# Kernel tuning notes

Hardware: AMD Instinct MI355X
Metric: run time of the kernel (lower is better)

## Reference

```python
import jax, jax.numpy as jnp
import numpy as np

D = 1024; H = 16; N = 64; F = 4096
B = 1; T = 2048
W_LORA = 64; A_LORA = 64; V_LORA = 32; G_LORA = 128


def rmsnorm(x, w, eps=1e-6):
    x32 = x.astype(jnp.float32)
    var = jnp.mean(x32 * x32, axis=-1, keepdims=True)
    return w * (x32 * jax.lax.rsqrt(var + eps))


def rwkv7_scan(r, w_log, k, v, a, b, state):
    # r,w_log,k,v,a,b: [B,T,H,N]; state: [B,H,N,N] (value dim, key dim)
    decay = jnp.exp(w_log)  # kernel applies exp to the log-decay w = -exp(w_pre)
    def step(S, inp):
        r_t, d_t, k_t, v_t, a_t, b_t = inp  # each [B,H,N]
        sa = jnp.einsum('bhij,bhj->bhi', S, a_t)
        S = S * d_t[:, :, None, :] + sa[..., None] * b_t[:, :, None, :] + v_t[..., None] * k_t[:, :, None, :]
        o_t = jnp.einsum('bhij,bhj->bhi', S, r_t)
        return S, o_t
    seq = tuple(jnp.moveaxis(t, 1, 0) for t in (r, decay, k, v, a, b))  # [T,B,H,N]
    state_f, o = jax.lax.scan(step, state, seq)
    return jnp.moveaxis(o, 0, 1), state_f  # [B,T,H,N], [B,H,N,N]


def setup_inputs() -> dict:
    key = jax.random.key(0)
    ks = iter(jax.random.split(key, 64))
    def nrm(shape, s=1.0):
        return jax.random.normal(next(ks), shape, dtype=jnp.float32) * s
    def uni(shape):
        return jax.random.uniform(next(ks), shape, dtype=jnp.float32)
    WS = 0.02  # weight scale for big matrices
    inp = {
        'x': nrm((B, T, D)),
        'x_prev': nrm((B, D)),
        'v_first': nrm((B, T, D)),
        'state': jnp.zeros((B, H, N, N), jnp.float32),
        'ln1_w': jnp.ones((D,), jnp.float32),
        'ln2_w': jnp.ones((D,), jnp.float32),
        'x_r': uni((1, 1, D)), 'x_w': uni((1, 1, D)), 'x_k': uni((1, 1, D)),
        'x_v': uni((1, 1, D)), 'x_a': uni((1, 1, D)), 'x_g': uni((1, 1, D)),
        'w0': nrm((1, 1, D), 0.5), 'w1': nrm((D, W_LORA), WS), 'w2': nrm((W_LORA, D), WS),
        'a0': nrm((1, 1, D), 0.1), 'a1': nrm((D, A_LORA), WS), 'a2': nrm((A_LORA, D), WS),
        'v0': nrm((1, 1, D), 0.1), 'v1': nrm((D, V_LORA), WS), 'v2': nrm((V_LORA, D), WS),
        'g1': nrm((D, G_LORA), WS), 'g2': nrm((G_LORA, D), WS),
        'k_k': uni((D,)), 'k_a': uni((D,)), 'r_k': nrm((D,), 0.1),
        'R_': nrm((D, D), WS), 'K_': nrm((D, D), WS), 'V_': nrm((D, D), WS), 'O_': nrm((D, D), WS),
        'gate_w': nrm((D, F), WS), 'up_w': nrm((D, F), WS), 'down_w': nrm((F, D), WS),
    }
    return inp


def _block(x, x_prev, v_first, state, ln1_w, ln2_w, x_r, x_w, x_k, x_v, x_a, x_g,
           w0, w1, w2, a0, a1, a2, v0, v1, v2, g1, g2, k_k, k_a, r_k,
           R_, K_, V_, O_, gate_w, up_w, down_w):
    Bx, Tx, _ = x.shape
    xn = rmsnorm(x, ln1_w)  # ln1
    # token shift
    xx = jnp.concatenate([x_prev[:, None, :], xn[:, :-1]], axis=1) - xn
    xr = xn + xx * x_r; xw = xn + xx * x_w; xk = xn + xx * x_k
    xv = xn + xx * x_v; xa = xn + xx * x_a; xg = xn + xx * x_g
    r = xr @ R_
    w_pre = -jax.nn.softplus(-(w0 + jnp.tanh(xw @ w1) @ w2)) - 0.5
    k = xk @ K_
    v = xv @ V_
    a = jax.nn.sigmoid(a0 + (xa @ a1) @ a2)
    g = jax.nn.sigmoid(xg @ g1) @ g2
    kk = (k * k_k).reshape(Bx, Tx, H, N)
    kk = kk / jnp.maximum(jnp.linalg.norm(kk, axis=-1, keepdims=True), 1e-12)
    kk = kk.reshape(Bx, Tx, H * N)
    k = k * (1 + (a - 1) * k_a)
    # layer_id > 0: lerp toward v_first
    v = v + (v_first - v) * jax.nn.sigmoid(v0 + (xv @ v1) @ v2)
    w_log = -jnp.exp(w_pre)  # log-decay passed to the recurrent kernel
    aa = -kk
    bb = kk * a
    hv = lambda t: t.reshape(Bx, Tx, H, N)
    o, state_f = rwkv7_scan(hv(r), hv(w_log), hv(k), hv(v), hv(aa), hv(bb), state)
    o = o.reshape(Bx, Tx, H * N)
    bonus = ((r * k * r_k).reshape(Bx, Tx, H, N).sum(-1, keepdims=True) * v.reshape(Bx, Tx, H, N)).reshape(Bx, Tx, H * N)
    o = o + bonus
    x = x + (o * g) @ O_
    # SwiGLU MLP
    xm = rmsnorm(x, ln2_w)
    x = x + (jax.nn.silu(xm @ gate_w) * (xm @ up_w)) @ down_w
    return x, xn[:, -1], state_f


def reference(x, x_prev, v_first, state, ln1_w, ln2_w, x_r, x_w, x_k, x_v, x_a, x_g,
              w0, w1, w2, a0, a1, a2, v0, v1, v2, g1, g2, k_k, k_a, r_k,
              R_, K_, V_, O_, gate_w, up_w, down_w):
    return _block(x, x_prev, v_first, state, ln1_w, ln2_w, x_r, x_w, x_k, x_v, x_a, x_g,
                  w0, w1, w2, a0, a1, a2, v0, v1, v2, g1, g2, k_k, k_a, r_k,
                  R_, K_, V_, O_, gate_w, up_w, down_w)
```

## Files before the change

kernel.cpp:

```cpp
#include <hip/hip_runtime.h>
#include <math.h>

#define T_ 2048
#define D_ 1024
#define H_ 16
#define N_ 64
#define F_ 4096
#define NCHUNK 64
#define CLEN 32

typedef __attribute__((ext_vector_type(8))) short bf16x8;
typedef __attribute__((ext_vector_type(4))) float f32x4;
typedef __attribute__((address_space(3))) unsigned int lds_u32_t;
typedef __attribute__((address_space(1))) const unsigned int glb_u32_t;

static __device__ __forceinline__ float sigf(float x) { return 1.0f / (1.0f + __expf(-x)); }

static __device__ __forceinline__ ushort f2bf(float f) {
    union { float f; unsigned u; } c; c.f = f;
    unsigned r = (c.u + 0x7FFFu + ((c.u >> 16) & 1u)) >> 16;
    return (ushort)r;
}
static __device__ __forceinline__ float bf2f(ushort h) {
    union { unsigned u; float f; } c; c.u = ((unsigned)h) << 16;
    return c.f;
}

static __device__ __forceinline__ void st4(float* p, float4 v) { *(float4*)p = v; }
static __device__ __forceinline__ void st4(ushort* p, float4 v) {
    ushort4 o; o.x = f2bf(v.x); o.y = f2bf(v.y); o.z = f2bf(v.z); o.w = f2bf(v.w);
    *(ushort4*)p = o;
}

template <typename OutT>
__global__ __launch_bounds__(256) void rmsnorm_kernel(const float* __restrict__ x,
                                                      const float* __restrict__ w,
                                                      OutT* __restrict__ out,
                                                      float* __restrict__ last) {
    const int t = blockIdx.x;
    const int tid = threadIdx.x;
    const float4* xr = (const float4*)(x + (size_t)t * D_);
    float4 v = xr[tid];
    float ss = v.x * v.x + v.y * v.y + v.z * v.z + v.w * v.w;
    ss += __shfl_xor(ss, 1);
    ss += __shfl_xor(ss, 2);
    ss += __shfl_xor(ss, 4);
    ss += __shfl_xor(ss, 8);
    ss += __shfl_xor(ss, 16);
    ss += __shfl_xor(ss, 32);
    __shared__ float red[4];
    if ((tid & 63) == 0) red[tid >> 6] = ss;
    __syncthreads();
    float tot = red[0] + red[1] + red[2] + red[3];
    float scale = rsqrtf(tot * (1.0f / (float)D_) + 1e-6f);
    float4 wv = ((const float4*)w)[tid];
    float4 o;
    o.x = wv.x * v.x * scale;
    o.y = wv.y * v.y * scale;
    o.z = wv.z * v.z * scale;
    o.w = wv.w * v.w * scale;
    st4(out + (size_t)t * D_ + tid * 4, o);
    if (last != nullptr && t == T_ - 1) ((float4*)last)[tid] = o;
}

__global__ __launch_bounds__(256) void rmsnorm_reduce2(
    const float* __restrict__ x, const float* __restrict__ p0, const float* __restrict__ p1,
    const float* __restrict__ w, float* __restrict__ resid_out, ushort* __restrict__ xm) {
    const int t = blockIdx.x;
    const int tid = threadIdx.x;
    const size_t base = (size_t)t * D_ + tid * 4;
    float4 v = *(const float4*)(x + base);
    float4 a = *(const float4*)(p0 + base);
    float4 b = *(const float4*)(p1 + base);
    v.x += a.x + b.x; v.y += a.y + b.y; v.z += a.z + b.z; v.w += a.w + b.w;
    st4(resid_out + base, v);
    float ss = v.x * v.x + v.y * v.y + v.z * v.z + v.w * v.w;
    ss += __shfl_xor(ss, 1);
    ss += __shfl_xor(ss, 2);
    ss += __shfl_xor(ss, 4);
    ss += __shfl_xor(ss, 8);
    ss += __shfl_xor(ss, 16);
    ss += __shfl_xor(ss, 32);
    __shared__ float red[4];
    if ((tid & 63) == 0) red[tid >> 6] = ss;
    __syncthreads();
    float tot = red[0] + red[1] + red[2] + red[3];
    float scale = rsqrtf(tot * (1.0f / (float)D_) + 1e-6f);
    float4 wv = ((const float4*)w)[tid];
    float4 o;
    o.x = wv.x * v.x * scale;
    o.y = wv.y * v.y * scale;
    o.z = wv.z * v.z * scale;
    o.w = wv.w * v.w * scale;
    st4(xm + base, o);
}

__global__ __launch_bounds__(256) void add4_kernel(float* __restrict__ out,
                                                   const float* __restrict__ p,
                                                   int n4slice) {
    const int i = blockIdx.x * 256 + threadIdx.x;
    const float4* p4 = (const float4*)p;
    float4 o = ((const float4*)out)[i];
    float4 a = p4[i], b = p4[i + n4slice], c = p4[i + 2 * n4slice], d = p4[i + 3 * n4slice];
    o.x += (a.x + b.x) + (c.x + d.x);
    o.y += (a.y + b.y) + (c.y + d.y);
    o.z += (a.z + b.z) + (c.z + d.z);
    o.w += (a.w + b.w) + (c.w + d.w);
    ((float4*)out)[i] = o;
}

__global__ __launch_bounds__(256) void shift_kernel(
    const float* __restrict__ xn, const float* __restrict__ x_prev,
    const float* __restrict__ cr, const float* __restrict__ cw, const float* __restrict__ ck,
    const float* __restrict__ cv, const float* __restrict__ ca, const float* __restrict__ cg,
    ushort* __restrict__ xr, ushort* __restrict__ xw, ushort* __restrict__ xk,
    ushort* __restrict__ xv, ushort* __restrict__ xa, ushort* __restrict__ xg) {
    const int i = blockIdx.x * 256 + threadIdx.x;
    const int t = i >> 8, j = i & 255;
    const float4* xn4 = (const float4*)xn;
    float4 cur = xn4[i];
    float4 prev = (t == 0) ? ((const float4*)x_prev)[j] : xn4[i - 256];
    float4 xx;
    xx.x = prev.x - cur.x;
    xx.y = prev.y - cur.y;
    xx.z = prev.z - cur.z;
    xx.w = prev.w - cur.w;
#define APPLY(dst, c)                                   \
    {                                                   \
        float4 cc = ((const float4*)c)[j];              \
        float4 o;                                       \
        o.x = cur.x + xx.x * cc.x;                      \
        o.y = cur.y + xx.y * cc.y;                      \
        o.z = cur.z + xx.z * cc.z;                      \
        o.w = cur.w + xx.w * cc.w;                      \
        st4(dst + (size_t)i * 4, o);                    \
    }
    APPLY(xr, cr)
    APPLY(xw, cw)
    APPLY(xk, ck)
    APPLY(xv, cv)
    APPLY(xa, ca)
    APPLY(xg, cg)
#undef APPLY
}

struct TDesc { const float* in; ushort* out; int K, N, off; };
struct TPack { TDesc d[15]; };

__global__ __launch_bounds__(256) void transpose_cast_multi(TPack p) {
    __shared__ float tile[32][33];
    const int bid = blockIdx.x;
    int di = 0;
#pragma unroll
    for (int i = 1; i < 15; i++)
        if (bid >= p.d[i].off) di = i;
    const TDesc d = p.d[di];
    const int local = bid - d.off;
    const int nt = d.N >> 5;
    const int bx = local % nt, by = local / nt;
    const int tx = threadIdx.x & 31, ty = threadIdx.x >> 5;
    const int n0 = bx * 32, k0 = by * 32;
#pragma unroll
    for (int i = 0; i < 4; i++)
        tile[ty + i * 8][tx] = d.in[(size_t)(k0 + ty + i * 8) * d.N + n0 + tx];
    __syncthreads();
#pragma unroll
    for (int i = 0; i < 4; i++)
        d.out[(size_t)(n0 + ty + i * 8) * d.K + k0 + tx] = f2bf(tile[tx][ty + i * 8]);
}

template <typename OutT, bool PARTIAL>
__global__ __launch_bounds__(256) void mfma_gemm(
    const ushort* __restrict__ A, const ushort* __restrict__ BT, OutT* __restrict__ C,
    const float* res, int M, int Ntot, int K, int klen, int epi) {
    __shared__ ushort As[2][128 * 32];
    __shared__ ushort Bs[2][128 * 32];
    const int tid = threadIdx.x;
    const int wave = tid >> 6, lane = tid & 63;
    const int wr = wave >> 1, wc = wave & 1;
    const int lrow = lane & 15, quad = lane >> 4;
    int bx = blockIdx.x, by = blockIdx.y;
    if (gridDim.x == 8 && gridDim.y == 16) {
        const int bid = by * 8 + bx;
        const int k = bid & 7, i = bid >> 3;
        bx = ((k & 1) << 2) + (i & 3);
        by = ((k >> 1) << 2) + (i >> 2);
    }
    const int m0 = by * 128, n0 = bx * 128;
    const int kbase = blockIdx.z * klen;
    const int srow = lane >> 2;
    const int scol = (lane & 3) << 3;

    f32x4 acc[4][4] = {};

    auto stage = [&](int buf, int kk) {
#pragma unroll
        for (int j = 0; j < 2; j++) {
            const int chunk = 2 * wave + j;
            const ushort* ga = A + (size_t)(m0 + chunk * 16 + srow) * K + kk + scol;
            __builtin_amdgcn_global_load_lds((glb_u32_t*)ga,
                                             (lds_u32_t*)&As[buf][chunk * 512], 16, 0, 0);
            const int brow = n0 + chunk * 16 + srow;
            if (brow < Ntot) {
                const ushort* gb = BT + (size_t)brow * K + kk + scol;
                __builtin_amdgcn_global_load_lds((glb_u32_t*)gb,
                                                 (lds_u32_t*)&Bs[buf][chunk * 512], 16, 0, 0);
            }
        }
    };

    stage(0, kbase);
    __syncthreads();
    int cur = 0;
    for (int k0 = kbase; k0 < kbase + klen; k0 += 32) {
        if (k0 + 32 < kbase + klen) stage(cur ^ 1, k0 + 32);
        bf16x8 af[4], bfr[4];
#pragma unroll
        for (int mi = 0; mi < 4; mi++)
            af[mi] = *(const bf16x8*)&As[cur][(wr * 64 + mi * 16 + lrow) * 32 + quad * 8];
#pragma unroll
        for (int ni = 0; ni < 4; ni++)
            bfr[ni] = *(const bf16x8*)&Bs[cur][(wc * 64 + ni * 16 + lrow) * 32 + quad * 8];
#pragma unroll
        for (int mi = 0; mi < 4; mi++)
#pragma unroll
            for (int ni = 0; ni < 4; ni++)
                acc[mi][ni] = __builtin_amdgcn_mfma_f32_16x16x32_bf16(af[mi], bfr[ni], acc[mi][ni], 0, 0, 0);
        __syncthreads();
        cur ^= 1;
    }

    const size_t zoff = PARTIAL ? (size_t)blockIdx.z * M * Ntot : 0;
#pragma unroll
    for (int mi = 0; mi < 4; mi++) {
#pragma unroll
        for (int r = 0; r < 4; r++) {
            const int row = m0 + wr * 64 + mi * 16 + quad * 4 + r;
#pragma unroll
            for (int ni = 0; ni < 4; ni++) {
                const int col = n0 + wc * 64 + ni * 16 + lrow;
                if (col < Ntot) {
                    const size_t idx = (size_t)row * Ntot + col;
                    float val = acc[mi][ni][r];
                    if constexpr (PARTIAL) {
                        ((float*)C)[idx + zoff] = val;
                    } else {
                        if (epi == 1) val += res[idx];
                        if constexpr (sizeof(OutT) == 2) C[idx] = (OutT)f2bf(val);
                        else C[idx] = (OutT)val;
                    }
                }
            }
        }
    }
}

struct MMDesc {
    const ushort* A; const ushort* BT;
    float* Cf; ushort* Cb;
    const float* res; const float* res2; const float* bias;
    int Ntot, K, epi;
};
template <int NZ>
struct MMPack { MMDesc d[NZ]; };

template <int NZ>
__global__ __launch_bounds__(256) void mfma_gemm_multi(MMPack<NZ> p) {
    const MMDesc d = p.d[blockIdx.z];
    const int n0 = blockIdx.x * 128;
    if (n0 >= d.Ntot) return;
    __shared__ ushort As[2][128 * 32];
    __shared__ ushort Bs[2][128 * 32];
    const int tid = threadIdx.x;
    const int wave = tid >> 6, lane = tid & 63;
    const int wr = wave >> 1, wc = wave & 1;
    const int lrow = lane & 15, quad = lane >> 4;
    const int m0 = blockIdx.y * 128;
    const int srow = lane >> 2;
    const int scol = (lane & 3) << 3;
    const int K = d.K, Ntot = d.Ntot;

    f32x4 acc[4][4] = {};

    auto stage = [&](int buf, int kk) {
#pragma unroll
        for (int j = 0; j < 2; j++) {
            const int chunk = 2 * wave + j;
            const ushort* ga = d.A + (size_t)(m0 + chunk * 16 + srow) * K + kk + scol;
            __builtin_amdgcn_global_load_lds((glb_u32_t*)ga,
                                             (lds_u32_t*)&As[buf][chunk * 512], 16, 0, 0);
            const int brow = n0 + chunk * 16 + srow;
            if (brow < Ntot) {
                const ushort* gb = d.BT + (size_t)brow * K + kk + scol;
                __builtin_amdgcn_global_load_lds((glb_u32_t*)gb,
                                                 (lds_u32_t*)&Bs[buf][chunk * 512], 16, 0, 0);
            }
        }
    };

    stage(0, 0);
    __syncthreads();
    int cur = 0;
    for (int k0 = 0; k0 < K; k0 += 32) {
        if (k0 + 32 < K) stage(cur ^ 1, k0 + 32);
        bf16x8 af[4], bfr[4];
#pragma unroll
        for (int mi = 0; mi < 4; mi++)
            af[mi] = *(const bf16x8*)&As[cur][(wr * 64 + mi * 16 + lrow) * 32 + quad * 8];
#pragma unroll
        for (int ni = 0; ni < 4; ni++)
            bfr[ni] = *(const bf16x8*)&Bs[cur][(wc * 64 + ni * 16 + lrow) * 32 + quad * 8];
#pragma unroll
        for (int mi = 0; mi < 4; mi++)
#pragma unroll
            for (int ni = 0; ni < 4; ni++)
                acc[mi][ni] = __builtin_amdgcn_mfma_f32_16x16x32_bf16(af[mi], bfr[ni], acc[mi][ni], 0, 0, 0);
        __syncthreads();
        cur ^= 1;
    }

#pragma unroll
    for (int mi = 0; mi < 4; mi++) {
#pragma unroll
        for (int r = 0; r < 4; r++) {
            const int row = m0 + wr * 64 + mi * 16 + quad * 4 + r;
#pragma unroll
            for (int ni = 0; ni < 4; ni++) {
                const int col = n0 + wc * 64 + ni * 16 + lrow;
                if (col < Ntot) {
                    const size_t idx = (size_t)row * Ntot + col;
                    float val = acc[mi][ni][r];
                    switch (d.epi) {
                        case 3: val = tanhf(val); break;
                        case 4: val = sigf(val); break;
                        case 5: val = sigf(d.bias[col] + val); break;
                        case 6: val = __expf(-0.60653065971263342f * sigf(d.bias[col] + val)); break;
                        case 7: {
                            float vr = d.res[idx];
                            val = vr + (d.res2[idx] - vr) * sigf(d.bias[col] + val);
                        } break;
                        default: break;
                    }
                    if (d.Cb) d.Cb[idx] = f2bf(val);
                    else d.Cf[idx] = val;
                }
            }
        }
    }
}

__global__ __launch_bounds__(256) void kk_kernel(float* __restrict__ k,
                                                 const float* __restrict__ a_sig,
                                                 const float* __restrict__ k_k,
                                                 const float* __restrict__ k_a,
                                                 float* __restrict__ kk,
                                                 float* __restrict__ mb) {
    const int b = blockIdx.x * 4 + (threadIdx.x >> 6);
    const int t = b >> 4, h = b & 15;
    const int lane = threadIdx.x & 63;
    const size_t idx = (size_t)t * D_ + h * N_ + lane;
    const int wi = h * N_ + lane;
    const float kraw = k[idx];
    const float kv = kraw * k_k[wi];
    float ss = kv * kv;
    ss += __shfl_xor(ss, 1);
    ss += __shfl_xor(ss, 2);
    ss += __shfl_xor(ss, 4);
    ss += __shfl_xor(ss, 8);
    ss += __shfl_xor(ss, 16);
    ss += __shfl_xor(ss, 32);
    const float nrm = fmaxf(sqrtf(ss), 1e-12f);
    const float kkn = kv / nrm;
    kk[idx] = kkn;
    mb[idx] = -kkn * a_sig[idx];
    k[idx] = kraw * (1.0f + (a_sig[idx] - 1.0f) * k_a[wi]);
}

#define FOR16(M) M(0) M(1) M(2) M(3) M(4) M(5) M(6) M(7) \
                 M(8) M(9) M(10) M(11) M(12) M(13) M(14) M(15)

__global__ __launch_bounds__(64, 1) void scan_pass1(
    const float* __restrict__ gR, const float* __restrict__ gD, const float* __restrict__ gK,
    const float* __restrict__ gV, const float* __restrict__ gKK, const float* __restrict__ gMB,
    float* __restrict__ Pbuf, float* __restrict__ Lbuf,
    float* __restrict__ zbuf, float* __restrict__ olbuf) {
    const int bid = blockIdx.x;
    const int h = bid & 15;
    const int c = bid >> 4;
    const int lane = threadIdx.x;
    const int hb = h * N_;
    const int t0 = c * CLEN;
    const int tend = t0 + CLEN - 1;

    __shared__ __align__(16) unsigned char ring[2 * 2048];

    const int rsel = lane >> 4;
    const int sub4 = (lane & 15) << 2;
    const float* p1 = (rsel == 0 ? gR : rsel == 1 ? gD : rsel == 2 ? gK : gKK)
                      + (size_t)t0 * D_ + hb + sub4;
    const float* p2 = (rsel == 1 ? gV : gMB) + (size_t)t0 * D_ + hb + sub4;

#define DECLP(q) f32x4 sp##q = {(lane == 4 * q + 0) ? 1.0f : 0.0f, \
                                (lane == 4 * q + 1) ? 1.0f : 0.0f, \
                                (lane == 4 * q + 2) ? 1.0f : 0.0f, \
                                (lane == 4 * q + 3) ? 1.0f : 0.0f};
    FOR16(DECLP)
#undef DECLP
#define DECLL(q) f32x4 sl##q = {0.f, 0.f, 0.f, 0.f};
    FOR16(DECLL)
#undef DECLL

    float4 r0a, r0b, r1a, r1b, r2a, r2b, r3a, r3b;

#define LOADQ(qa, qb, tt) {                                                  \
        const size_t _adv = (size_t)((tt) - t0) * D_;                        \
        qa = *(const float4*)(p1 + _adv);                                    \
        qb = *(const float4*)(p2 + _adv); }
#define WRITEQ(sl, qa, qb) {                                                 \
        *(float4*)(ring + (sl) * 2048 + lane * 16) = qa;                     \
        *(float4*)(ring + (sl) * 2048 + 1024 + lane * 16) = qb; }
#define PA(q) { const f32x4 kk4 = sKKr[q];                                   \
        pacc += sp##q * kk4; lacc += sl##q * kk4; }
#define PB(q) {                                                   \
        const f32x4 d4 = sDr[q];                                  \
        const f32x4 k4 = sKr[q];                                  \
        const f32x4 m4 = sMBr[q];                                 \
        const f32x4 r4 = sRr[q];                                  \
        sp##q = sp##q * d4 + m4 * sapP;                           \
        sl##q = sl##q * d4 + (m4 * sapL + k4 * vv);               \
        oP += sp##q * r4;                                         \
        oL += sl##q * r4;                                         \
    }
#define COMPUTE(sl, tt) {                                                    \
        const unsigned char* sb = (const unsigned char*)ring + (sl) * 2048;  \
        const f32x4* sRr = (const f32x4*)(sb);                               \
        const f32x4* sDr = (const f32x4*)(sb + 256);                         \
        const f32x4* sKr = (const f32x4*)(sb + 512);                         \
        const f32x4* sKKr = (const f32x4*)(sb + 768);                        \
        const f32x4* sMBr = (const f32x4*)(sb + 1024);                       \
        const float* sVr = (const float*)(sb + 1280);                        \
        f32x4 pacc = {0.f, 0.f, 0.f, 0.f};                                   \
        f32x4 lacc = {0.f, 0.f, 0.f, 0.f};                                   \
        FOR16(PA)                                                            \
        const float sapP = (pacc.x + pacc.y) + (pacc.z + pacc.w);            \
        const float sapL = (lacc.x + lacc.y) + (lacc.z + lacc.w);            \
        const float vv = sVr[lane];                                          \
        f32x4 oP = {0.f, 0.f, 0.f, 0.f};                                     \
        f32x4 oL = {0.f, 0.f, 0.f, 0.f};                                     \
        FOR16(PB)                                                            \
        zbuf[(size_t)(tt) * D_ + hb + lane] = (oP.x + oP.y) + (oP.z + oP.w); \
        olbuf[(size_t)(tt) * D_ + hb + lane] = (oL.x + oL.y) + (oL.z + oL.w); }

    LOADQ(r0a, r0b, t0)
    LOADQ(r1a, r1b, t0 + 1)
    LOADQ(r2a, r2b, t0 + 2)
    LOADQ(r3a, r3b, t0 + 3)
    WRITEQ(0, r0a, r0b)

    for (int t = t0; t < t0 + CLEN; t += 4) {
        WRITEQ(1, r1a, r1b)
        LOADQ(r0a, r0b, (t + 4 > tend ? tend : t + 4))
        COMPUTE(0, t)
        WRITEQ(0, r2a, r2b)
        LOADQ(r1a, r1b, (t + 5 > tend ? tend : t + 5))
        COMPUTE(1, t + 1)
        WRITEQ(1, r3a, r3b)
        LOADQ(r2a, r2b, (t + 6 > tend ? tend : t + 6))
        COMPUTE(0, t + 2)
        WRITEQ(0, r0a, r0b)
        LOADQ(r3a, r3b, (t + 7 > tend ? tend : t + 7))
        COMPUTE(1, t + 3)
    }
#undef COMPUTE
#undef PB
#undef PA
#undef WRITEQ
#undef LOADQ

    const size_t base = ((size_t)c * 16 + h) * 4096 + (size_t)lane * 64;
#define STP(q) *(f32x4*)(Pbuf + base + 4 * q) = sp##q;
    FOR16(STP)
#undef STP
#define STL(q) *(f32x4*)(Lbuf + base + 4 * q) = sl##q;
    FOR16(STL)
#undef STL
}

__global__ __launch_bounds__(64) void merge_pairs(float* __restrict__ Pbuf,
                                                  float* __restrict__ Lbuf) {
    const int h = blockIdx.x & 15, j = blockIdx.x >> 4;
    const int t = threadIdx.x;
    __shared__ float PaT[64][65];
    __shared__ float LaT[64][65];
    __shared__ float Pb[64][68];
    const size_t ca = ((size_t)(2 * j) * 16 + h) * 4096;
    const size_t cb = ((size_t)(2 * j + 1) * 16 + h) * 4096;
#pragma unroll
    for (int q = 0; q < 16; q++) {
        const int idx = t + q * 64;
        const int r = idx >> 4, c4 = (idx & 15) << 2;
        float4 pa = *(const float4*)(Pbuf + ca + (size_t)r * 64 + c4);
        float4 la = *(const float4*)(Lbuf + ca + (size_t)r * 64 + c4);
        float4 pb = *(const float4*)(Pbuf + cb + (size_t)r * 64 + c4);
        PaT[c4 + 0][r] = pa.x; PaT[c4 + 1][r] = pa.y;
        PaT[c4 + 2][r] = pa.z; PaT[c4 + 3][r] = pa.w;
        LaT[c4 + 0][r] = la.x; LaT[c4 + 1][r] = la.y;
        LaT[c4 + 2][r] = la.z; LaT[c4 + 3][r] = la.w;
        *(float4*)&Pb[r][c4] = pb;
    }
    __syncthreads();
    const int cg = (t & 3) << 4;
    const int r0 = (t >> 2) << 2;
    float4 accP[4][4] = {};
    float4 accL[4][4];
#pragma unroll
    for (int rr = 0; rr < 4; rr++)
#pragma unroll
        for (int e = 0; e < 4; e++)
            accL[rr][e] = *(const float4*)(Lbuf + cb + (size_t)(r0 + rr) * 64 + cg + 4 * e);
    for (int m = 0; m < 64; m++) {
        float4 pb4[4];
#pragma unroll
        for (int e = 0; e < 4; e++) pb4[e] = *(const float4*)&Pb[m][cg + 4 * e];
#pragma unroll
        for (int rr = 0; rr < 4; rr++) {
            const float pa = PaT[m][r0 + rr];
            const float la = LaT[m][r0 + rr];
#pragma unroll
            for (int e = 0; e < 4; e++) {
                accP[rr][e].x = fmaf(pa, pb4[e].x, accP[rr][e].x);
                accP[rr][e].y = fmaf(pa, pb4[e].y, accP[rr][e].y);
                accP[rr][e].z = fmaf(pa, pb4[e].z, accP[rr][e].z);
                accP[rr][e].w = fmaf(pa, pb4[e].w, accP[rr][e].w);
                accL[rr][e].x = fmaf(la, pb4[e].x, accL[rr][e].x);
                accL[rr][e].y = fmaf(la, pb4[e].y, accL[rr][e].y);
                accL[rr][e].z = fmaf(la, pb4[e].z, accL[rr][e].z);
                accL[rr][e].w = fmaf(la, pb4[e].w, accL[rr][e].w);
            }
        }
    }
#pragma unroll
    for (int rr = 0; rr < 4; rr++)
#pragma unroll
        for (int e = 0; e < 4; e++) {
            *(float4*)(Pbuf + cb + (size_t)(r0 + rr) * 64 + cg + 4 * e) = accP[rr][e];
            *(float4*)(Lbuf + cb + (size_t)(r0 + rr) * 64 + cg + 4 * e) = accL[rr][e];
        }
}

__global__ __launch_bounds__(256) void scan_combine(
    const float* __restrict__ state_in, const float* __restrict__ Pbuf,
    const float* __restrict__ Lbuf, float* __restrict__ SstT, float* __restrict__ state_out) {
    const int h = blockIdx.x >> 2, rg = blockIdx.x & 3;
    const int tid = threadIdx.x;
    const int i = tid >> 4, j4 = (tid & 15) << 2;
    const int gi = rg * 16 + i;
    __shared__ float Sl[16][68];
    __shared__ float Pl[64][68];

    float4 sv = *(const float4*)(state_in + (size_t)h * 4096 + gi * 64 + j4);
    *(float4*)&Sl[i][j4] = sv;

    float4 rp0, rp1, rp2, rp3, rl;
    {
        const size_t cb = ((size_t)1 * 16 + h) * 4096;
        rp0 = *(const float4*)(Pbuf + cb + (size_t)(i +  0) * 64 + j4);
        rp1 = *(const float4*)(Pbuf + cb + (size_t)(i + 16) * 64 + j4);
        rp2 = *(const float4*)(Pbuf + cb + (size_t)(i + 32) * 64 + j4);
        rp3 = *(const float4*)(Pbuf + cb + (size_t)(i + 48) * 64 + j4);
        rl  = *(const float4*)(Lbuf + cb + (size_t)gi * 64 + j4);
    }
    __syncthreads();

    for (int c = 0; c < NCHUNK / 2; c++) {
        *(float4*)&Pl[i +  0][j4] = rp0;
        *(float4*)&Pl[i + 16][j4] = rp1;
        *(float4*)&Pl[i + 32][j4] = rp2;
        *(float4*)&Pl[i + 48][j4] = rp3;
        float4 acc = rl;
        const size_t so = ((size_t)(2 * c) * 16 + h) * 4096;
        float4 scur = *(const float4*)&Sl[i][j4];
        SstT[so + (size_t)(j4 + 0) * 64 + gi] = scur.x;
        SstT[so + (size_t)(j4 + 1) * 64 + gi] = scur.y;
        SstT[so + (size_t)(j4 + 2) * 64 + gi] = scur.z;
        SstT[so + (size_t)(j4 + 3) * 64 + gi] = scur.w;
        __syncthreads();
        if (c + 1 < NCHUNK / 2) {
            const size_t cb = ((size_t)(2 * c + 3) * 16 + h) * 4096;
            rp0 = *(const float4*)(Pbuf + cb + (size_t)(i +  0) * 64 + j4);
            rp1 = *(const float4*)(Pbuf + cb + (size_t)(i + 16) * 64 + j4);
            rp2 = *(const float4*)(Pbuf + cb + (size_t)(i + 32) * 64 + j4);
            rp3 = *(const float4*)(Pbuf + cb + (size_t)(i + 48) * 64 + j4);
            rl  = *(const float4*)(Lbuf + cb + (size_t)gi * 64 + j4);
        }
#pragma unroll 8
        for (int m = 0; m < 64; m++) {
            const float smv = Sl[i][m];
            const float4 p4 = *(const float4*)&Pl[m][j4];
            acc.x = fmaf(smv, p4.x, acc.x);
            acc.y = fmaf(smv, p4.y, acc.y);
            acc.z = fmaf(smv, p4.z, acc.z);
            acc.w = fmaf(smv, p4.w, acc.w);
        }
        __syncthreads();
        *(float4*)&Sl[i][j4] = acc;
    }
    *(float4*)(state_out + (size_t)h * 4096 + gi * 64 + j4) = *(const float4*)&Sl[i][j4];
}

__global__ __launch_bounds__(256) void scan_oddfill(
    const float* __restrict__ Pbuf, const float* __restrict__ Lbuf,
    float* __restrict__ SstT) {
    const int b = blockIdx.x;
    const int rg = b & 3, h = (b >> 2) & 15, j = b >> 6;
    const int tid = threadIdx.x;
    const int i = tid >> 4, j4 = (tid & 15) << 2;
    const int gi = rg * 16 + i;
    __shared__ float Sl[16][68];
    __shared__ float Pl[64][68];
    const size_t ce = ((size_t)(2 * j) * 16 + h) * 4096;
    const size_t co = ((size_t)(2 * j + 1) * 16 + h) * 4096;
    {
        float4 s;
        s.x = SstT[ce + (size_t)(j4 + 0) * 64 + gi];
        s.y = SstT[ce + (size_t)(j4 + 1) * 64 + gi];
        s.z = SstT[ce + (size_t)(j4 + 2) * 64 + gi];
        s.w = SstT[ce + (size_t)(j4 + 3) * 64 + gi];
        *(float4*)&Sl[i][j4] = s;
    }
#pragma unroll
    for (int q = 0; q < 4; q++) {
        const int prq = i + q * 16;
        *(float4*)&Pl[prq][j4] = *(const float4*)(Pbuf + ce + (size_t)prq * 64 + j4);
    }
    __syncthreads();
    float4 acc = *(const float4*)(Lbuf + ce + (size_t)gi * 64 + j4);
#pragma unroll 8
    for (int m = 0; m < 64; m++) {
        const float smv = Sl[i][m];
        const float4 p4 = *(const float4*)&Pl[m][j4];
        acc.x = fmaf(smv, p4.x, acc.x);
        acc.y = fmaf(smv, p4.y, acc.y);
        acc.z = fmaf(smv, p4.z, acc.z);
        acc.w = fmaf(smv, p4.w, acc.w);
    }
    SstT[co + (size_t)(j4 + 0) * 64 + gi] = acc.x;
    SstT[co + (size_t)(j4 + 1) * 64 + gi] = acc.y;
    SstT[co + (size_t)(j4 + 2) * 64 + gi] = acc.z;
    SstT[co + (size_t)(j4 + 3) * 64 + gi] = acc.w;
}

__global__ __launch_bounds__(256) void scan_fix(
    const float* __restrict__ zbuf, const float* __restrict__ olbuf,
    const float* __restrict__ SstT, float* __restrict__ o) {
    const int tg = blockIdx.x >> 4, h = blockIdx.x & 15;
    const int hb = h * N_;
    const int tid = threadIdx.x;
    const int tok = tid >> 4, i4 = (tid & 15) << 2;
    const int tbase = tg * 16;
    const int c = tbase / CLEN;
    __shared__ float zl[16][68];
    __shared__ float Sl[64][68];

    *(float4*)&zl[tok][i4] = *(const float4*)(zbuf + (size_t)(tbase + tok) * D_ + hb + i4);
    const size_t cb = ((size_t)c * 16 + h) * 4096;
#pragma unroll
    for (int q = 0; q < 4; q++) {
        const int jr = (tid >> 4) + q * 16;
        *(float4*)&Sl[jr][i4] = *(const float4*)(SstT + cb + (size_t)jr * 64 + i4);
    }
    __syncthreads();
    float4 acc = *(const float4*)(olbuf + (size_t)(tbase + tok) * D_ + hb + i4);
#pragma unroll 8
    for (int j = 0; j < 64; j++) {
        const float zv = zl[tok][j];
        const float4 p4 = *(const float4*)&Sl[j][i4];
        acc.x = fmaf(zv, p4.x, acc.x);
        acc.y = fmaf(zv, p4.y, acc.y);
        acc.z = fmaf(zv, p4.z, acc.z);
        acc.w = fmaf(zv, p4.w, acc.w);
    }
    *(float4*)(o + (size_t)(tbase + tok) * D_ + hb + i4) = acc;
}

__global__ __launch_bounds__(256) void bonus_kernel(const float* __restrict__ o,
                                                    const float* __restrict__ r,
                                                    const float* __restrict__ k,
                                                    const float* __restrict__ v,
                                                    const float* __restrict__ g,
                                                    const float* __restrict__ r_k,
                                                    ushort* __restrict__ og) {
    const int b = blockIdx.x * 4 + (threadIdx.x >> 6);
    const int t = b >> 4, h = b & 15;
    const int lane = threadIdx.x & 63;
    const size_t idx = (size_t)t * D_ + h * N_ + lane;
    float c = r[idx] * k[idx] * r_k[h * N_ + lane];
    c += __shfl_xor(c, 1);
    c += __shfl_xor(c, 2);
    c += __shfl_xor(c, 4);
    c += __shfl_xor(c, 8);
    c += __shfl_xor(c, 16);
    c += __shfl_xor(c, 32);
    const float on = o[idx] + c * v[idx];
    og[idx] = f2bf(on * g[idx]);
}

__global__ __launch_bounds__(256) void mulz_kernel(const ushort* __restrict__ Z,
                                                   ushort* __restrict__ Hb) {
    const int idx = blockIdx.x * 256 + threadIdx.x;
    const int t = idx >> 10;
    const int j = (idx & 1023) << 2;
    const ushort4 zg = *(const ushort4*)(Z + (size_t)t * 8192 + j);
    const ushort4 zu = *(const ushort4*)(Z + (size_t)t * 8192 + 4096 + j);
    ushort4 o;
    float g0 = bf2f(zg.x), g1 = bf2f(zg.y), g2 = bf2f(zg.z), g3 = bf2f(zg.w);
    o.x = f2bf(g0 * sigf(g0) * bf2f(zu.x));
    o.y = f2bf(g1 * sigf(g1) * bf2f(zu.y));
    o.z = f2bf(g2 * sigf(g2) * bf2f(zu.z));
    o.w = f2bf(g3 * sigf(g3) * bf2f(zu.w));
    *(ushort4*)(Hb + (size_t)t * 4096 + j) = o;
}

extern "C" void kernel_launch(void* const* d_in, const int* in_sizes, int n_in,
                              void* d_out, int out_size, void* d_ws, size_t ws_size,
                              hipStream_t stream) {
    const float* x      = (const float*)d_in[0];
    const float* x_prev = (const float*)d_in[1];
    const float* v_first= (const float*)d_in[2];
    const float* state  = (const float*)d_in[3];
    const float* ln1_w  = (const float*)d_in[4];
    const float* ln2_w  = (const float*)d_in[5];
    const float* x_r    = (const float*)d_in[6];
    const float* x_w    = (const float*)d_in[7];
    const float* x_k    = (const float*)d_in[8];
    const float* x_v    = (const float*)d_in[9];
    const float* x_a    = (const float*)d_in[10];
    const float* x_g    = (const float*)d_in[11];
    const float* w0     = (const float*)d_in[12];
    const float* w1     = (const float*)d_in[13];
    const float* w2     = (const float*)d_in[14];
    const float* a0     = (const float*)d_in[15];
    const float* a1     = (const float*)d_in[16];
    const float* a2     = (const float*)d_in[17];
    const float* v0     = (const float*)d_in[18];
    const float* v1     = (const float*)d_in[19];
    const float* v2     = (const float*)d_in[20];
    const float* g1     = (const float*)d_in[21];
    const float* g2     = (const float*)d_in[22];
    const float* k_k    = (const float*)d_in[23];
    const float* k_a    = (const float*)d_in[24];
    const float* r_k    = (const float*)d_in[25];
    const float* R_     = (const float*)d_in[26];
    const float* K_     = (const float*)d_in[27];
    const float* V_     = (const float*)d_in[28];
    const float* O_     = (const float*)d_in[29];
    const float* gate_w = (const float*)d_in[30];
    const float* up_w   = (const float*)d_in[31];
    const float* down_w = (const float*)d_in[32];

    float* ws = (float*)d_ws;
    const size_t U = (size_t)T_ * D_;
    float* u_r  = ws;
    float* u_k  = ws + 1 * U;
    float* u_v  = ws + 2 * U;
    float* u_dc = ws + 3 * U;
    float* u_kk = ws + 4 * U;
    float* u_mb = ws + 5 * U;
    float* u_g  = ws + 6 * U;
    float* u_ao = ws + 7 * U;
    ushort* XB = (ushort*)(ws + 8 * U);
    const size_t TD = U;
    ushort* XR = XB + 0 * TD;
    ushort* XW = XB + 1 * TD;
    ushort* XK = XB + 2 * TD;
    ushort* XV = XB + 3 * TD;
    ushort* XA = XB + 4 * TD;
    ushort* XG = XB + 5 * TD;
    float* Pbuf  = (float*)XB;
    float* Lbuf  = u_g;
    float* zbuf  = ws + 10 * U;
    float* olbuf = (float*)d_out;
    float* SstT  = u_dc;
    float* obuf  = u_mb;
    ushort* OG   = XB;
    ushort* XM   = (ushort*)(ws + 10 * U);
    float* Opart = ws + 4 * U;
    ushort* Zbuf = (ushort*)ws;
    ushort* Hbuf = (ushort*)(ws + 4 * U);
    float* Dpart = ws;
    ushort* WT = (ushort*)(ws + 11 * U);
    const size_t DD = (size_t)D_ * D_;
    const size_t DF = (size_t)D_ * F_;
    ushort* WTR = WT;
    ushort* WTK = WTR + DD;
    ushort* WTV = WTK + DD;
    ushort* WTO = WTV + DD;
    ushort* WTG = WTO + DD;
    ushort* WTU = WTG + DF;
    ushort* WTD = WTU + DF;
    ushort* WTw1 = WTD + DF;
    ushort* WTw2 = WTw1 + 64 * 1024;
    ushort* WTa1 = WTw2 + 64 * 1024;
    ushort* WTa2 = WTa1 + 64 * 1024;
    ushort* WTv1 = WTa2 + 64 * 1024;
    ushort* WTv2 = WTv1 + 32 * 1024;
    ushort* WTg1 = WTv2 + 32 * 1024;
    ushort* WTg2 = WTg1 + 128 * 1024;
    ushort* Lw = WTg2 + 128 * 1024;
    ushort* La = Lw + (size_t)T_ * 64;
    ushort* Lv = La + (size_t)T_ * 64;
    ushort* Lg = Lv + (size_t)T_ * 32;

    float* out_x = (float*)d_out;
    float* out_xn_last = out_x + (size_t)T_ * D_;
    float* out_state = out_xn_last + D_;

    TPack tp;
    int toff = 0, ti = 0;
    auto addT = [&](const float* in, ushort* out, int K, int N) {
        tp.d[ti].in = in; tp.d[ti].out = out; tp.d[ti].K = K; tp.d[ti].N = N; tp.d[ti].off = toff;
        toff += (N / 32) * (K / 32); ++ti;
    };
    addT(R_, WTR, D_, D_);
    addT(K_, WTK, D_, D_);
    addT(V_, WTV, D_, D_);
    addT(O_, WTO, D_, D_);
    addT(gate_w, WTG, D_, F_);
    addT(up_w, WTU, D_, F_);
    addT(down_w, WTD, F_, D_);
    addT(w1, WTw1, D_, 64);
    addT(w2, WTw2, 64, D_);
    addT(a1, WTa1, D_, 64);
    addT(a2, WTa2, 64, D_);
    addT(v1, WTv1, D_, 32);
    addT(v2, WTv2, 32, D_);
    addT(g1, WTg1, D_, 128);
    addT(g2, WTg2, 128, D_);
    transpose_cast_multi<<<toff, 256, 0, stream>>>(tp);

    rmsnorm_kernel<float><<<T_, 256, 0, stream>>>(x, ln1_w, out_x, out_xn_last);
    shift_kernel<<<T_, 256, 0, stream>>>(out_x, x_prev, x_r, x_w, x_k, x_v, x_a, x_g,
                                         XR, XW, XK, XV, XA, XG);
    auto mkmm = [](const ushort* A, const ushort* BT, float* Cf, ushort* Cb,
                   const float* res, const float* res2, const float* bias,
                   int Ntot, int K, int epi) {
        MMDesc m{A, BT, Cf, Cb, res, res2, bias, Ntot, K, epi};
        return m;
    };
    MMPack<7> pa;
    pa.d[0] = mkmm(XR, WTR, u_r, nullptr, nullptr, nullptr, nullptr, D_, D_, 0);
    pa.d[1] = mkmm(XK, WTK, u_k, nullptr, nullptr, nullptr, nullptr, D_, D_, 0);
    pa.d[2] = mkmm(XV, WTV, u_v, nullptr, nullptr, nullptr, nullptr, D_, D_, 0);
    pa.d[3] = mkmm(XW, WTw1, nullptr, Lw, nullptr, nullptr, nullptr, 64,  D_, 3);
    pa.d[4] = mkmm(XA, WTa1, nullptr, La, nullptr, nullptr, nullptr, 64,  D_, 0);
    pa.d[5] = mkmm(XV, WTv1, nullptr, Lv, nullptr, nullptr, nullptr, 32,  D_, 0);
    pa.d[6] = mkmm(XG, WTg1, nullptr, Lg, nullptr, nullptr, nullptr, 128, D_, 4);
    mfma_gemm_multi<7><<<dim3(8, 16, 7), 256, 0, stream>>>(pa);
    MMPack<3> pb;
    pb.d[0] = mkmm(Lw, WTw2, u_dc, nullptr, nullptr, nullptr, w0, D_, 64,  6);
    pb.d[1] = mkmm(La, WTa2, u_ao, nullptr, nullptr, nullptr, a0, D_, 64,  5);
    pb.d[2] = mkmm(Lv, WTv2, u_v,  nullptr, u_v, v_first,     v0, D_, 32,  7);
    mfma_gemm_multi<3><<<dim3(8, 16, 3), 256, 0, stream>>>(pb);
    kk_kernel<<<T_ * H_ / 4, 256, 0, stream>>>(u_k, u_ao, k_k, k_a, u_kk, u_mb);
    scan_pass1<<<NCHUNK * H_, 64, 0, stream>>>(u_r, u_dc, u_k, u_v, u_kk, u_mb,
                                               Pbuf, Lbuf, zbuf, olbuf);
    merge_pairs<<<16 * 32, 64, 0, stream>>>(Pbuf, Lbuf);
    scan_combine<<<H_ * 4, 256, 0, stream>>>(state, Pbuf, Lbuf, SstT, out_state);
    scan_oddfill<<<16 * 32 * 4, 256, 0, stream>>>(Pbuf, Lbuf, SstT);
    mfma_gemm<float, false><<<dim3(8, 16), 256, 0, stream>>>(
        Lg, WTg2, u_g, nullptr, T_, D_, 128, 128, 0);
    scan_fix<<<(T_ / 16) * H_, 256, 0, stream>>>(zbuf, olbuf, SstT, obuf);
    bonus_kernel<<<T_ * H_ / 4, 256, 0, stream>>>(obuf, u_r, u_k, u_v, u_g, r_k, OG);
    mfma_gemm<float, true><<<dim3(8, 16, 2), 256, 0, stream>>>(
        OG, WTO, Opart, nullptr, T_, D_, D_, 512, 0);
    rmsnorm_reduce2<<<T_, 256, 0, stream>>>(x, Opart, Opart + U, ln2_w, out_x, XM);
    mfma_gemm<ushort, false><<<dim3(64, 16), 256, 0, stream>>>(
        XM, WTG, Zbuf, nullptr, T_, 2 * F_, D_, D_, 0);
    mulz_kernel<<<(T_ * (F_ / 4)) / 256, 256, 0, stream>>>(Zbuf, Hbuf);
    mfma_gemm<float, true><<<dim3(8, 16, 4), 256, 0, stream>>>(
        Hbuf, WTD, Dpart, nullptr, T_, D_, F_, 1024, 0);
    add4_kernel<<<(int)(U / 4 / 256), 256, 0, stream>>>(out_x, Dpart, (int)(U / 4));
}
```

Measured before the change: 620.1 us.

## Fuse rmsnorm with token shift, bonus into scan_fix, and SwiGLU into GEMM epilogue

Merges the first rmsnorm and the token-shift kernel into one kernel that recomputes the previous token's norm instead of reading it back. The bonus/gating pass moves into scan_fix, and the gate/up weights are interleaved in 16-column groups so the fused gate-up GEMM can apply silu(g)*u in its epilogue and write the hidden activations directly. This removes three launches and the round trips through the large intermediate Z buffer and the o buffer, at the cost of doing the previous-row norm twice and a more involved GEMM epilogue and weight layout.

Result: no change. 612.6 us (-1.2%).

```diff
diff --git a/kernel.cpp b/kernel.cpp
--- a/kernel.cpp
+++ b/kernel.cpp
@@ -32,35 +32,66 @@
     *(ushort4*)p = o;
 }
 
-template <typename OutT>
-__global__ __launch_bounds__(256) void rmsnorm_kernel(const float* __restrict__ x,
-                                                      const float* __restrict__ w,
-                                                      OutT* __restrict__ out,
-                                                      float* __restrict__ last) {
+__global__ __launch_bounds__(256) void ln_shift_kernel(
+    const float* __restrict__ x, const float* __restrict__ x_prev,
+    const float* __restrict__ w,
+    const float* __restrict__ cr, const float* __restrict__ cw, const float* __restrict__ ck,
+    const float* __restrict__ cv, const float* __restrict__ ca, const float* __restrict__ cg,
+    ushort* __restrict__ xr, ushort* __restrict__ xw, ushort* __restrict__ xk,
+    ushort* __restrict__ xv, ushort* __restrict__ xa, ushort* __restrict__ xg,
+    float* __restrict__ last) {
     const int t = blockIdx.x;
     const int tid = threadIdx.x;
-    const float4* xr = (const float4*)(x + (size_t)t * D_);
-    float4 v = xr[tid];
-    float ss = v.x * v.x + v.y * v.y + v.z * v.z + v.w * v.w;
-    ss += __shfl_xor(ss, 1);
-    ss += __shfl_xor(ss, 2);
-    ss += __shfl_xor(ss, 4);
-    ss += __shfl_xor(ss, 8);
-    ss += __shfl_xor(ss, 16);
-    ss += __shfl_xor(ss, 32);
-    __shared__ float red[4];
-    if ((tid & 63) == 0) red[tid >> 6] = ss;
+    const float4* x4 = (const float4*)x;
+    float4 xc = x4[t * 256 + tid];
+    float4 xp = (t == 0) ? ((const float4*)x_prev)[tid] : x4[(t - 1) * 256 + tid];
+    float ssc = xc.x * xc.x + xc.y * xc.y + xc.z * xc.z + xc.w * xc.w;
+    float ssp = xp.x * xp.x + xp.y * xp.y + xp.z * xp.z + xp.w * xp.w;
+    ssc += __shfl_xor(ssc, 1); ssp += __shfl_xor(ssp, 1);
+    ssc += __shfl_xor(ssc, 2); ssp += __shfl_xor(ssp, 2);
+    ssc += __shfl_xor(ssc, 4); ssp += __shfl_xor(ssp, 4);
+    ssc += __shfl_xor(ssc, 8); ssp += __shfl_xor(ssp, 8);
+    ssc += __shfl_xor(ssc, 16); ssp += __shfl_xor(ssp, 16);
+    ssc += __shfl_xor(ssc, 32); ssp += __shfl_xor(ssp, 32);
+    __shared__ float redc[4], redp[4];
+    if ((tid & 63) == 0) { redc[tid >> 6] = ssc; redp[tid >> 6] = ssp; }
     __syncthreads();
-    float tot = red[0] + red[1] + red[2] + red[3];
-    float scale = rsqrtf(tot * (1.0f / (float)D_) + 1e-6f);
+    const float totc = redc[0] + redc[1] + redc[2] + redc[3];
+    const float totp = redp[0] + redp[1] + redp[2] + redp[3];
+    const float sc = rsqrtf(totc * (1.0f / (float)D_) + 1e-6f);
+    const float sp = rsqrtf(totp * (1.0f / (float)D_) + 1e-6f);
     float4 wv = ((const float4*)w)[tid];
-    float4 o;
-    o.x = wv.x * v.x * scale;
-    o.y = wv.y * v.y * scale;
-    o.z = wv.z * v.z * scale;
-    o.w = wv.w * v.w * scale;
-    st4(out + (size_t)t * D_ + tid * 4, o);
-    if (last != nullptr && t == T_ - 1) ((float4*)last)[tid] = o;
+    float4 cur, prev;
+    cur.x = wv.x * xc.x * sc; cur.y = wv.y * xc.y * sc;
+    cur.z = wv.z * xc.z * sc; cur.w = wv.w * xc.w * sc;
+    if (t == 0) {
+        prev = xp;
+    } else {
+        prev.x = wv.x * xp.x * sp; prev.y = wv.y * xp.y * sp;
+        prev.z = wv.z * xp.z * sp; prev.w = wv.w * xp.w * sp;
+    }
+    float4 xx;
+    xx.x = prev.x - cur.x; xx.y = prev.y - cur.y;
+    xx.z = prev.z - cur.z; xx.w = prev.w - cur.w;
+    const size_t ob = (size_t)t * D_ + tid * 4;
+#define APPLY(dst, c)                                   \
+    {                                                   \
+        float4 cc = ((const float4*)c)[tid];            \
+        float4 o;                                       \
+        o.x = cur.x + xx.x * cc.x;                      \
+        o.y = cur.y + xx.y * cc.y;                      \
+        o.z = cur.z + xx.z * cc.z;                      \
+        o.w = cur.w + xx.w * cc.w;                      \
+        st4(dst + ob, o);                               \
+    }
+    APPLY(xr, cr)
+    APPLY(xw, cw)
+    APPLY(xk, ck)
+    APPLY(xv, cv)
+    APPLY(xa, ca)
+    APPLY(xg, cg)
+#undef APPLY
+    if (t == T_ - 1) ((float4*)last)[tid] = cur;
 }
 
 __global__ __launch_bounds__(256) void rmsnorm_reduce2(
@@ -109,42 +140,7 @@
     ((float4*)out)[i] = o;
 }
 
-__global__ __launch_bounds__(256) void shift_kernel(
-    const float* __restrict__ xn, const float* __restrict__ x_prev,
-    const float* __restrict__ cr, const float* __restrict__ cw, const float* __restrict__ ck,
-    const float* __restrict__ cv, const float* __restrict__ ca, const float* __restrict__ cg,
-    ushort* __restrict__ xr, ushort* __restrict__ xw, ushort* __restrict__ xk,
-    ushort* __restrict__ xv, ushort* __restrict__ xa, ushort* __restrict__ xg) {
-    const int i = blockIdx.x * 256 + threadIdx.x;
-    const int t = i >> 8, j = i & 255;
-    const float4* xn4 = (const float4*)xn;
-    float4 cur = xn4[i];
-    float4 prev = (t == 0) ? ((const float4*)x_prev)[j] : xn4[i - 256];
-    float4 xx;
-    xx.x = prev.x - cur.x;
-    xx.y = prev.y - cur.y;
-    xx.z = prev.z - cur.z;
-    xx.w = prev.w - cur.w;
-#define APPLY(dst, c)                                   \
-    {                                                   \
-        float4 cc = ((const float4*)c)[j];              \
-        float4 o;                                       \
-        o.x = cur.x + xx.x * cc.x;                      \
-        o.y = cur.y + xx.y * cc.y;                      \
-        o.z = cur.z + xx.z * cc.z;                      \
-        o.w = cur.w + xx.w * cc.w;                      \
-        st4(dst + (size_t)i * 4, o);                    \
-    }
-    APPLY(xr, cr)
-    APPLY(xw, cw)
-    APPLY(xk, ck)
-    APPLY(xv, cv)
-    APPLY(xa, ca)
-    APPLY(xg, cg)
-#undef APPLY
-}
-
-struct TDesc { const float* in; ushort* out; int K, N, off; };
+struct TDesc { const float* in; ushort* out; int K, N, off, mode; };
 struct TPack { TDesc d[15]; };
 
 __global__ __launch_bounds__(256) void transpose_cast_multi(TPack p) {
@@ -165,8 +161,13 @@
         tile[ty + i * 8][tx] = d.in[(size_t)(k0 + ty + i * 8) * d.N + n0 + tx];
     __syncthreads();
 #pragma unroll
-    for (int i = 0; i < 4; i++)
-        d.out[(size_t)(n0 + ty + i * 8) * d.K + k0 + tx] = f2bf(tile[tx][ty + i * 8]);
+    for (int i = 0; i < 4; i++) {
+        const int n = n0 + ty + i * 8;
+        int ro = n;
+        if (d.mode == 1) ro = ((n >> 4) << 5) + (n & 15);
+        else if (d.mode == 2) ro = ((n >> 4) << 5) + 16 + (n & 15);
+        d.out[(size_t)ro * d.K + k0 + tx] = f2bf(tile[tx][ty + i * 8]);
+    }
 }
 
 template <typename OutT, bool PARTIAL>
@@ -231,11 +232,25 @@
     }
 
     const size_t zoff = PARTIAL ? (size_t)blockIdx.z * M * Ntot : 0;
+    const int hstride = Ntot >> 1;
 #pragma unroll
     for (int mi = 0; mi < 4; mi++) {
 #pragma unroll
         for (int r = 0; r < 4; r++) {
             const int row = m0 + wr * 64 + mi * 16 + quad * 4 + r;
+            if (epi == 2) {
+                if constexpr (!PARTIAL && sizeof(OutT) == 2) {
+#pragma unroll
+                    for (int ni = 0; ni < 4; ni += 2) {
+                        const int ci = n0 + wc * 64 + ni * 16 + lrow;
+                        const float gv = acc[mi][ni][r];
+                        const float uv = acc[mi][ni + 1][r];
+                        const int co = ((ci >> 5) << 4) + (ci & 15);
+                        C[(size_t)row * hstride + co] = (OutT)f2bf(gv * sigf(gv) * uv);
+                    }
+                }
+                continue;
+            }
 #pragma unroll
             for (int ni = 0; ni < 4; ni++) {
                 const int col = n0 + wc * 64 + ni * 16 + lrow;
@@ -652,7 +667,10 @@
 
 __global__ __launch_bounds__(256) void scan_fix(
     const float* __restrict__ zbuf, const float* __restrict__ olbuf,
-    const float* __restrict__ SstT, float* __restrict__ o) {
+    const float* __restrict__ SstT,
+    const float* __restrict__ r, const float* __restrict__ k,
+    const float* __restrict__ v, const float* __restrict__ g,
+    const float* __restrict__ r_k, ushort* __restrict__ og) {
     const int tg = blockIdx.x >> 4, h = blockIdx.x & 15;
     const int hb = h * N_;
     const int tid = threadIdx.x;
@@ -670,7 +688,8 @@
         *(float4*)&Sl[jr][i4] = *(const float4*)(SstT + cb + (size_t)jr * 64 + i4);
     }
     __syncthreads();
-    float4 acc = *(const float4*)(olbuf + (size_t)(tbase + tok) * D_ + hb + i4);
+    const size_t tix = (size_t)(tbase + tok) * D_ + hb + i4;
+    float4 acc = *(const float4*)(olbuf + tix);
 #pragma unroll 8
     for (int j = 0; j < 64; j++) {
         const float zv = zl[tok][j];
@@ -680,45 +699,23 @@
         acc.z = fmaf(zv, p4.z, acc.z);
         acc.w = fmaf(zv, p4.w, acc.w);
     }
-    *(float4*)(o + (size_t)(tbase + tok) * D_ + hb + i4) = acc;
-}
-
-__global__ __launch_bounds__(256) void bonus_kernel(const float* __restrict__ o,
-                                                    const float* __restrict__ r,
-                                                    const float* __restrict__ k,
-                                                    const float* __restrict__ v,
-                                                    const float* __restrict__ g,
-                                                    const float* __restrict__ r_k,
-                                                    ushort* __restrict__ og) {
-    const int b = blockIdx.x * 4 + (threadIdx.x >> 6);
-    const int t = b >> 4, h = b & 15;
-    const int lane = threadIdx.x & 63;
-    const size_t idx = (size_t)t * D_ + h * N_ + lane;
-    float c = r[idx] * k[idx] * r_k[h * N_ + lane];
-    c += __shfl_xor(c, 1);
-    c += __shfl_xor(c, 2);
-    c += __shfl_xor(c, 4);
-    c += __shfl_xor(c, 8);
-    c += __shfl_xor(c, 16);
-    c += __shfl_xor(c, 32);
-    const float on = o[idx] + c * v[idx];
-    og[idx] = f2bf(on * g[idx]);
-}
-
-__global__ __launch_bounds__(256) void mulz_kernel(const ushort* __restrict__ Z,
-                                                   ushort* __restrict__ Hb) {
-    const int idx = blockIdx.x * 256 + threadIdx.x;
-    const int t = idx >> 10;
-    const int j = (idx & 1023) << 2;
-    const ushort4 zg = *(const ushort4*)(Z + (size_t)t * 8192 + j);
-    const ushort4 zu = *(const ushort4*)(Z + (size_t)t * 8192 + 4096 + j);
-    ushort4 o;
-    float g0 = bf2f(zg.x), g1 = bf2f(zg.y), g2 = bf2f(zg.z), g3 = bf2f(zg.w);
-    o.x = f2bf(g0 * sigf(g0) * bf2f(zu.x));
-    o.y = f2bf(g1 * sigf(g1) * bf2f(zu.y));
-    o.z = f2bf(g2 * sigf(g2) * bf2f(zu.z));
-    o.w = f2bf(g3 * sigf(g3) * bf2f(zu.w));
-    *(ushort4*)(Hb + (size_t)t * 4096 + j) = o;
+    float4 rv = *(const float4*)(r + tix);
+    float4 kv = *(const float4*)(k + tix);
+    float4 rk = *(const float4*)(r_k + hb + i4);
+    float cc = rv.x * kv.x * rk.x + rv.y * kv.y * rk.y +
+               rv.z * kv.z * rk.z + rv.w * kv.w * rk.w;
+    cc += __shfl_xor(cc, 1);
+    cc += __shfl_xor(cc, 2);
+    cc += __shfl_xor(cc, 4);
+    cc += __shfl_xor(cc, 8);
+    float4 vv = *(const float4*)(v + tix);
+    float4 gv = *(const float4*)(g + tix);
+    float4 o;
+    o.x = (acc.x + cc * vv.x) * gv.x;
+    o.y = (acc.y + cc * vv.y) * gv.y;
+    o.z = (acc.z + cc * vv.z) * gv.z;
+    o.w = (acc.w + cc * vv.w) * gv.w;
+    st4(og + tix, o);
 }
 
 extern "C" void kernel_launch(void* const* d_in, const int* in_sizes, int n_in,
@@ -781,11 +778,9 @@
     float* zbuf  = ws + 10 * U;
     float* olbuf = (float*)d_out;
     float* SstT  = u_dc;
-    float* obuf  = u_mb;
     ushort* OG   = XB;
     ushort* XM   = (ushort*)(ws + 10 * U);
     float* Opart = ws + 4 * U;
-    ushort* Zbuf = (ushort*)ws;
     ushort* Hbuf = (ushort*)(ws + 4 * U);
     float* Dpart = ws;
     ushort* WT = (ushort*)(ws + 11 * U);
@@ -795,9 +790,8 @@
     ushort* WTK = WTR + DD;
     ushort* WTV = WTK + DD;
     ushort* WTO = WTV + DD;
-    ushort* WTG = WTO + DD;
-    ushort* WTU = WTG + DF;
-    ushort* WTD = WTU + DF;
+    ushort* WTGU = WTO + DD;
+    ushort* WTD = WTGU + 2 * DF;
     ushort* WTw1 = WTD + DF;
     ushort* WTw2 = WTw1 + 64 * 1024;
     ushort* WTa1 = WTw2 + 64 * 1024;
@@ -817,30 +811,31 @@
 
     TPack tp;
     int toff = 0, ti = 0;
-    auto addT = [&](const float* in, ushort* out, int K, int N) {
-        tp.d[ti].in = in; tp.d[ti].out = out; tp.d[ti].K = K; tp.d[ti].N = N; tp.d[ti].off = toff;
+    auto addT = [&](const float* in, ushort* out, int K, int N, int mode) {
+        tp.d[ti].in = in; tp.d[ti].out = out; tp.d[ti].K = K; tp.d[ti].N = N;
+        tp.d[ti].off = toff; tp.d[ti].mode = mode;
         toff += (N / 32) * (K / 32); ++ti;
     };
-    addT(R_, WTR, D_, D_);
-    addT(K_, WTK, D_, D_);
-    addT(V_, WTV, D_, D_);
-    addT(O_, WTO, D_, D_);
-    addT(gate_w, WTG, D_, F_);
-    addT(up_w, WTU, D_, F_);
-    addT(down_w, WTD, F_, D_);
-    addT(w1, WTw1, D_, 64);
-    addT(w2, WTw2, 64, D_);
-    addT(a1, WTa1, D_, 64);
-    addT(a2, WTa2, 64, D_);
-    addT(v1, WTv1, D_, 32);
-    addT(v2, WTv2, 32, D_);
-    addT(g1, WTg1, D_, 128);
-    addT(g2, WTg2, 128, D_);
+    addT(R_, WTR, D_, D_, 0);
+    addT(K_, WTK, D_, D_, 0);
+    addT(V_, WTV, D_, D_, 0);
+    addT(O_, WTO, D_, D_, 0);
+    addT(gate_w, WTGU, D_, F_, 1);
+    addT(up_w, WTGU, D_, F_, 2);
+    addT(down_w, WTD, F_, D_, 0);
+    addT(w1, WTw1, D_, 64, 0);
+    addT(w2, WTw2, 64, D_, 0);
+    addT(a1, WTa1, D_, 64, 0);
+    addT(a2, WTa2, 64, D_, 0);
+    addT(v1, WTv1, D_, 32, 0);
+    addT(v2, WTv2, 32, D_, 0);
+    addT(g1, WTg1, D_, 128, 0);
+    addT(g2, WTg2, 128, D_, 0);
     transpose_cast_multi<<<toff, 256, 0, stream>>>(tp);
 
-    rmsnorm_kernel<float><<<T_, 256, 0, stream>>>(x, ln1_w, out_x, out_xn_last);
-    shift_kernel<<<T_, 256, 0, stream>>>(out_x, x_prev, x_r, x_w, x_k, x_v, x_a, x_g,
-                                         XR, XW, XK, XV, XA, XG);
+    ln_shift_kernel<<<T_, 256, 0, stream>>>(x, x_prev, ln1_w,
+                                            x_r, x_w, x_k, x_v, x_a, x_g,
+                                            XR, XW, XK, XV, XA, XG, out_xn_last);
     auto mkmm = [](const ushort* A, const ushort* BT, float* Cf, ushort* Cb,
                    const float* res, const float* res2, const float* bias,
                    int Ntot, int K, int epi) {
@@ -869,14 +864,13 @@
     scan_oddfill<<<16 * 32 * 4, 256, 0, stream>>>(Pbuf, Lbuf, SstT);
     mfma_gemm<float, false><<<dim3(8, 16), 256, 0, stream>>>(
         Lg, WTg2, u_g, nullptr, T_, D_, 128, 128, 0);
-    scan_fix<<<(T_ / 16) * H_, 256, 0, stream>>>(zbuf, olbuf, SstT, obuf);
-    bonus_kernel<<<T_ * H_ / 4, 256, 0, stream>>>(obuf, u_r, u_k, u_v, u_g, r_k, OG);
+    scan_fix<<<(T_ / 16) * H_, 256, 0, stream>>>(zbuf, olbuf, SstT,
+                                                 u_r, u_k, u_v, u_g, r_k, OG);
     mfma_gemm<float, true><<<dim3(8, 16, 2), 256, 0, stream>>>(
         OG, WTO, Opart, nullptr, T_, D_, D_, 512, 0);
     rmsnorm_reduce2<<<T_, 256, 0, stream>>>(x, Opart, Opart + U, ln2_w, out_x, XM);
     mfma_gemm<ushort, false><<<dim3(64, 16), 256, 0, stream>>>(
-        XM, WTG, Zbuf, nullptr, T_, 2 * F_, D_, D_, 0);
-    mulz_kernel<<<(T_ * (F_ / 4)) / 256, 256, 0, stream>>>(Zbuf, Hbuf);
+        XM, WTGU, Hbuf, nullptr, T_, 2 * F_, D_, D_, 2);
     mfma_gemm<float, true><<<dim3(8, 16, 4), 256, 0, stream>>>(
         Hbuf, WTD, Dpart, nullptr, T_, D_, F_, 1024, 0);
     add4_kernel<<<(int)(U / 4 / 256), 256, 0, stream>>>(out_x, Dpart, (int)(U / 4));
```
